# Kernel optimization log

Hardware: AMD Instinct MI355X
Metric: run time of the kernel (lower is better)

Reference implementation:

```python
import jax, jax.numpy as jnp
import numpy as np
from jax import lax

B, ROWS, COLS, K, LATENT = 8, 1536, 16, 32, 16
EPS_REG = 0.01  # torchsort regularization_strength
BIG = 1e30


def setup_inputs() -> dict:
    key = jax.random.key(0)
    ks = jax.random.split(key, 12)
    def w(k, shape):
        return (jax.random.normal(k, shape, jnp.float32) / np.sqrt(shape[0])).astype(jnp.float32)
    return {
        "table": jax.random.uniform(ks[0], (B, ROWS, COLS), jnp.float32),
        "enc_w1": w(ks[1], (COLS, 32)), "enc_b1": 0.01 * jax.random.normal(ks[2], (32,), jnp.float32),
        "enc_w2": w(ks[3], (32, 64)),   "enc_b2": 0.01 * jax.random.normal(ks[4], (64,), jnp.float32),
        "mean_w": w(ks[5], (64, LATENT)), "mean_b": 0.01 * jax.random.normal(ks[6], (LATENT,), jnp.float32),
        "dec_w1": w(ks[7], (LATENT, 32)), "dec_b1": 0.01 * jax.random.normal(ks[8], (32,), jnp.float32),
        "dec_w2": w(ks[9], (32, COLS)),   "dec_b2": 0.01 * jax.random.normal(ks[10], (COLS,), jnp.float32),
        "labels": jax.random.randint(ks[11], (ROWS,), 0, K, jnp.int32),
        "BlockSize": 64,
        "current_epoch": 0,
        "baseline": 0,
    }


def _soft_rank_l2(s, eps):
    # Exact soft_rank (Blondel et al. / torchsort, l2 reg, ascending):
    # project s/eps onto permutahedron of (n,...,1).
    n = s.shape[0]
    x = s / eps
    perm = jnp.argsort(-x)            # descending sort
    xs = x[perm]
    w = jnp.arange(n, 0, -1, dtype=x.dtype)
    # dual = non-increasing isotonic fit of y = xs - w == -iso_inc(-(xs - w))
    y = -(xs - w)
    S = jnp.concatenate([jnp.zeros((1,), x.dtype), jnp.cumsum(y)])
    idx = jnp.arange(n)
    length = jnp.maximum(idx[None, :] - idx[:, None] + 1, 1).astype(x.dtype)
    A = (S[1:][None, :] - S[:n][:, None]) / length           # mean(y[j..k])  [j,k]
    A = jnp.where(idx[None, :] >= idx[:, None], A, BIG)
    Bm = lax.cummin(A, axis=1, reverse=True)                  # min_{k>=i} A[j,k]
    Cm = lax.cummax(Bm, axis=0)                               # max_{j<=i} ...
    iso_inc = jnp.diagonal(Cm)
    dual = -iso_inc
    primal = xs - dual
    inv = jnp.argsort(perm)
    return primal[inv]


def _forward(table, enc_w1, enc_b1, enc_w2, enc_b2, mean_w, mean_b,
             dec_w1, dec_b1, dec_w2, dec_b2, labels, BlockSize):
    b = table.shape[0]
    # VAE (autoencoder path; z = latent mean)
    h = jax.nn.relu(table @ enc_w1 + enc_b1)
    h = jax.nn.relu(h @ enc_w2 + enc_b2)
    z = h @ mean_w + mean_b                                   # [B, rows, 16]
    r = jax.nn.relu(z @ dec_w1 + dec_b1)
    recon = jax.nn.relu(r @ dec_w2 + dec_b2)
    loss = jnp.mean((recon - table) ** 2)
    # clustering scores (labels fixed from batch 0, shared across batch)
    onehot = jax.nn.one_hot(labels, K, dtype=z.dtype)         # [rows, K]
    counts = jnp.maximum(onehot.sum(0), 1.0)                  # [K]
    centers = jnp.einsum('brd,rk->bkd', z, onehot) / counts[None, :, None]
    center_data = centers[:, labels, :]                       # gather back [B, rows, 16]
    d2 = jnp.mean((z - center_data) ** 2, axis=-1)            # [B, rows]
    mn = d2.min(axis=1, keepdims=True); mx = d2.max(axis=1, keepdims=True)
    d2 = (d2 - mn) / (mx - mn)
    scores = d2 + labels.astype(z.dtype)[None, :]
    # training branch
    smn = scores.min(axis=1, keepdims=True); smx = scores.max(axis=1, keepdims=True)
    scaled = (scores - smn) / (smx - smn) * jnp.asarray(b, z.dtype)  # * len(table)
    ranks = jax.vmap(lambda s: _soft_rank_l2(s, EPS_REG))(scaled)
    rank_idx = jnp.argsort(jnp.argsort(scores, axis=1), axis=1) // BlockSize + 1
    rows = table.shape[1]
    return (ranks.reshape(b, rows, 1), rank_idx.reshape(b, rows, 1),
            scores.reshape(b, rows, 1), loss)


def reference(table, enc_w1, enc_b1, enc_w2, enc_b2, mean_w, mean_b,
              dec_w1, dec_b1, dec_w2, dec_b2, labels, BlockSize,
              current_epoch, baseline):
    return _forward(table, enc_w1, enc_b1, enc_w2, enc_b2, mean_w, mean_b,
                    dec_w1, dec_b1, dec_w2, dec_b2, labels, BlockSize)
```

## Files before the change

### kernel.cpp

```cpp
#include <hip/hip_runtime.h>

#define BATCH 8
#define ROWS 1536
#define KCLS 32
#define NTOT (BATCH*ROWS)
#define ELEMS (NTOT*16)
#define SSTRIDE 3073
#define BIGF 1.0e30f

enum : int {
  WS_Z     = 0,
  WS_XS    = WS_Z + NTOT*16,
  WS_S     = WS_XS + NTOT,
  WS_DESC  = WS_S + BATCH*SSTRIDE,
  WS_ASCP  = WS_DESC + NTOT,
  WS_DSCP  = WS_ASCP + 4*NTOT,
  WS_GPART = WS_DSCP + 4*NTOT,
  WS_LOSSP = WS_GPART + BATCH*96*512,
};
#define WS_CPART WS_GPART

#define LW1  0
#define LB1  512
#define LW2  544
#define LB2  2592
#define LMW  2656
#define LMB  3680
#define LDW1 3696
#define LDB1 4208
#define LDW2 4240
#define LDB2 4752
#define LTOT 4768

#define AX   0
#define AH1  16
#define AH2  48
#define AZ   112
#define AR1  128
#define AREC 144
#define ASTRIDE 164

#define RPB 16

template<int IN_BASE, int IN_N, int OUT_BASE, int OUT_PW, int OUT_TOT,
         int WOFF, int BOFF, bool RELU>
__device__ __forceinline__ void layerw(float* __restrict__ act,
                                       const float* __restrict__ wsh,
                                       int lrow, int fway)
{
  const int o0 = fway * OUT_PW;
  float a0[OUT_PW], a1[OUT_PW], a2[OUT_PW], a3[OUT_PW];
#pragma unroll
  for (int j = 0; j < OUT_PW; ++j) {
    a0[j] = wsh[BOFF + o0 + j];
    a1[j] = 0.f; a2[j] = 0.f; a3[j] = 0.f;
  }

  const float4* arow = reinterpret_cast<const float4*>(&act[lrow*ASTRIDE + IN_BASE]);
#pragma unroll
  for (int i4 = 0; i4 < IN_N/4; ++i4) {
    const float4 sv = arow[i4];
    const float* wp0 = &wsh[WOFF + (i4*4 + 0)*OUT_TOT + o0];
    const float* wp1 = &wsh[WOFF + (i4*4 + 1)*OUT_TOT + o0];
    const float* wp2 = &wsh[WOFF + (i4*4 + 2)*OUT_TOT + o0];
    const float* wp3 = &wsh[WOFF + (i4*4 + 3)*OUT_TOT + o0];
    if constexpr (OUT_PW == 1) {
      a0[0] = fmaf(sv.x, wp0[0], a0[0]);
      a1[0] = fmaf(sv.y, wp1[0], a1[0]);
      a2[0] = fmaf(sv.z, wp2[0], a2[0]);
      a3[0] = fmaf(sv.w, wp3[0], a3[0]);
    } else if constexpr (OUT_PW == 2) {
      const float2 w0 = *reinterpret_cast<const float2*>(wp0);
      const float2 w1 = *reinterpret_cast<const float2*>(wp1);
      const float2 w2 = *reinterpret_cast<const float2*>(wp2);
      const float2 w3 = *reinterpret_cast<const float2*>(wp3);
      a0[0] = fmaf(sv.x, w0.x, a0[0]); a0[1] = fmaf(sv.x, w0.y, a0[1]);
      a1[0] = fmaf(sv.y, w1.x, a1[0]); a1[1] = fmaf(sv.y, w1.y, a1[1]);
      a2[0] = fmaf(sv.z, w2.x, a2[0]); a2[1] = fmaf(sv.z, w2.y, a2[1]);
      a3[0] = fmaf(sv.w, w3.x, a3[0]); a3[1] = fmaf(sv.w, w3.y, a3[1]);
    } else {
#pragma unroll
      for (int q = 0; q < OUT_PW/4; ++q) {
        const float4 w0 = reinterpret_cast<const float4*>(wp0)[q];
        const float4 w1 = reinterpret_cast<const float4*>(wp1)[q];
        const float4 w2 = reinterpret_cast<const float4*>(wp2)[q];
        const float4 w3 = reinterpret_cast<const float4*>(wp3)[q];
        a0[q*4+0] = fmaf(sv.x, w0.x, a0[q*4+0]);
        a0[q*4+1] = fmaf(sv.x, w0.y, a0[q*4+1]);
        a0[q*4+2] = fmaf(sv.x, w0.z, a0[q*4+2]);
        a0[q*4+3] = fmaf(sv.x, w0.w, a0[q*4+3]);
        a1[q*4+0] = fmaf(sv.y, w1.x, a1[q*4+0]);
        a1[q*4+1] = fmaf(sv.y, w1.y, a1[q*4+1]);
        a1[q*4+2] = fmaf(sv.y, w1.z, a1[q*4+2]);
        a1[q*4+3] = fmaf(sv.y, w1.w, a1[q*4+3]);
        a2[q*4+0] = fmaf(sv.z, w2.x, a2[q*4+0]);
        a2[q*4+1] = fmaf(sv.z, w2.y, a2[q*4+1]);
        a2[q*4+2] = fmaf(sv.z, w2.z, a2[q*4+2]);
        a2[q*4+3] = fmaf(sv.z, w2.w, a2[q*4+3]);
        a3[q*4+0] = fmaf(sv.w, w3.x, a3[q*4+0]);
        a3[q*4+1] = fmaf(sv.w, w3.y, a3[q*4+1]);
        a3[q*4+2] = fmaf(sv.w, w3.z, a3[q*4+2]);
        a3[q*4+3] = fmaf(sv.w, w3.w, a3[q*4+3]);
      }
    }
  }

  float* orow = &act[lrow*ASTRIDE + OUT_BASE + o0];
  if constexpr (OUT_PW == 1) {
    float v = (a0[0] + a1[0]) + (a2[0] + a3[0]);
    orow[0] = RELU ? fmaxf(v, 0.f) : v;
  } else if constexpr (OUT_PW == 2) {
    float2 v;
    v.x = (a0[0] + a1[0]) + (a2[0] + a3[0]);
    v.y = (a0[1] + a1[1]) + (a2[1] + a3[1]);
    if (RELU) { v.x = fmaxf(v.x, 0.f); v.y = fmaxf(v.y, 0.f); }
    *reinterpret_cast<float2*>(orow) = v;
  } else {
#pragma unroll
    for (int q = 0; q < OUT_PW/4; ++q) {
      float4 v;
      v.x = (a0[q*4+0] + a1[q*4+0]) + (a2[q*4+0] + a3[q*4+0]);
      v.y = (a0[q*4+1] + a1[q*4+1]) + (a2[q*4+1] + a3[q*4+1]);
      v.z = (a0[q*4+2] + a1[q*4+2]) + (a2[q*4+2] + a3[q*4+2]);
      v.w = (a0[q*4+3] + a1[q*4+3]) + (a2[q*4+3] + a3[q*4+3]);
      if (RELU) {
        v.x = fmaxf(v.x, 0.f); v.y = fmaxf(v.y, 0.f);
        v.z = fmaxf(v.z, 0.f); v.w = fmaxf(v.w, 0.f);
      }
      reinterpret_cast<float4*>(orow)[q] = v;
    }
  }
}

__global__ __launch_bounds__(256, 4) void k1_ae(
    const float* __restrict__ table,
    const float* __restrict__ w1, const float* __restrict__ b1,
    const float* __restrict__ w2, const float* __restrict__ b2,
    const float* __restrict__ mw, const float* __restrict__ mb,
    const float* __restrict__ dw1, const float* __restrict__ db1,
    const float* __restrict__ dw2, const float* __restrict__ db2,
    const int* __restrict__ labels,
    float* __restrict__ ws)
{
  const int tid  = threadIdx.x;
  const int lrow = tid & (RPB-1);
  const int fway = tid >> 4;
  const int blk  = blockIdx.x;
  const int b    = blk / 96;
  const int ch   = blk % 96;

  __shared__ float wsh[LTOT];
  __shared__ float act[RPB * ASTRIDE];
  __shared__ int   lbl[RPB];
  __shared__ float lred[4];

  {
    float4* d4 = reinterpret_cast<float4*>(wsh);
#define CPY(off, src, nf4) \
    { const float4* p = reinterpret_cast<const float4*>(src); \
      for (int t = tid; t < (nf4); t += 256) d4[(off)/4 + t] = p[t]; }
    CPY(LW1,  w1,  128) CPY(LB1,  b1,  8)  CPY(LW2,  w2,  512)
    CPY(LB2,  b2,  16)  CPY(LMW,  mw,  256) CPY(LMB,  mb,  4)
    CPY(LDW1, dw1, 128) CPY(LDB1, db1, 8)  CPY(LDW2, dw2, 128)
    CPY(LDB2, db2, 4)
#undef CPY
    if (tid < RPB) lbl[tid] = labels[ch * RPB + tid];
    if (tid < RPB*4) {
      const float4 v = reinterpret_cast<const float4*>(table)[blk*(RPB*4) + tid];
      reinterpret_cast<float4*>(act)[(tid >> 2)*(ASTRIDE/4) + (tid & 3)] = v;
    }
  }
  __syncthreads();

  layerw<AX,  16, AH1, 2, 32, LW1,  LB1,  true >(act, wsh, lrow, fway);
  __syncthreads();
  layerw<AH1, 32, AH2, 4, 64, LW2,  LB2,  true >(act, wsh, lrow, fway);
  __syncthreads();
  layerw<AH2, 64, AZ,  1, 16, LMW,  LMB,  false>(act, wsh, lrow, fway);
  __syncthreads();

  if (tid < RPB*4) {
    const float4 zv =
      reinterpret_cast<const float4*>(act)[(tid >> 2)*(ASTRIDE/4) + (AZ/4) + (tid & 3)];
    reinterpret_cast<float4*>(ws + WS_Z)[blk*(RPB*4) + tid] = zv;
  }

  layerw<AZ,  16, AR1, 2, 32, LDW1, LDB1, true >(act, wsh, lrow, fway);
  __syncthreads();
  layerw<AR1, 32, AREC,1, 16, LDW2, LDB2, true >(act, wsh, lrow, fway);
  __syncthreads();

  {
    const float d = act[lrow*ASTRIDE + AREC + fway] - act[lrow*ASTRIDE + AX + fway];
    float ls = d * d;
    for (int off = 32; off > 0; off >>= 1) ls += __shfl_down(ls, off);
    if ((tid & 63) == 0) lred[tid >> 6] = ls;
    __syncthreads();
    if (tid == 0) ws[WS_LOSSP + blk] = (lred[0] + lred[1]) + (lred[2] + lred[3]);
  }

  {
    float a0 = 0.f, a1 = 0.f;
    const int d0 = tid & 15, k0 = tid >> 4;
    const int k1c = k0 + 16;
#pragma unroll
    for (int rr = 0; rr < RPB; ++rr) {
      const int lb = lbl[rr];
      const float zv = act[rr*ASTRIDE + AZ + d0];
      a0 += (lb == k0)  ? zv : 0.f;
      a1 += (lb == k1c) ? zv : 0.f;
    }
    ws[WS_CPART + (b*96 + ch)*512 + tid]       = a0;
    ws[WS_CPART + (b*96 + ch)*512 + 256 + tid] = a1;
  }
}

__global__ __launch_bounds__(256) void kcount(const int* __restrict__ labels,
                                              float* __restrict__ ws,
                                              float* __restrict__ out)
{
  const int bi = blockIdx.x;
  const int jb = bi & 3, rb = (bi >> 2) % 6, b = bi / 24;
  const int tid = threadIdx.x;

  alignas(16) __shared__ float s_l[ROWS];
  __shared__ float cent[512];
  __shared__ float rmn[256], rmx[256];
  __shared__ int cnt[KCLS];

  if (tid < KCLS) cnt[tid] = 0;
  __syncthreads();

  int lbv[6];
#pragma unroll
  for (int c = 0; c < 6; ++c) {
    lbv[c] = labels[c*256 + tid];
    atomicAdd(&cnt[lbv[c]], 1);
  }

  float s1a = 0.f, s1b = 0.f, s2a = 0.f, s2b = 0.f;
  {
    const float* cp = ws + WS_CPART + (b*96)*512;
#pragma unroll 4
    for (int c = 0; c < 96; c += 2) {
      s1a += cp[c*512 + tid];
      s1b += cp[(c+1)*512 + tid];
      s2a += cp[c*512 + 256 + tid];
      s2b += cp[(c+1)*512 + 256 + tid];
    }
  }
  __syncthreads();
  {
    int cn1 = cnt[tid >> 4];         cn1 = cn1 > 1 ? cn1 : 1;
    int cn2 = cnt[(tid + 256) >> 4]; cn2 = cn2 > 1 ? cn2 : 1;
    cent[tid]       = (s1a + s1b) / (float)cn1;
    cent[tid + 256] = (s2a + s2b) / (float)cn2;
  }
  __syncthreads();

  float dv[6];
  float tmn = 3.0e38f, tmx = -3.0e38f;
#pragma unroll
  for (int c = 0; c < 6; ++c) {
    const int r = c*256 + tid;
    const float4* zp = reinterpret_cast<const float4*>(ws + WS_Z + (b*ROWS + r)*16);
    const float4* cq = reinterpret_cast<const float4*>(&cent[lbv[c]*16]);
    float s = 0.f;
#pragma unroll
    for (int q = 0; q < 4; ++q) {
      float4 zv = zp[q], cv = cq[q];
      float d0 = zv.x - cv.x, d1 = zv.y - cv.y, d2_ = zv.z - cv.z, d3 = zv.w - cv.w;
      s += d0*d0 + d1*d1 + d2_*d2_ + d3*d3;
    }
    dv[c] = s / 16.f;
    tmn = fminf(tmn, dv[c]); tmx = fmaxf(tmx, dv[c]);
  }
  rmn[tid] = tmn; rmx[tid] = tmx;
  __syncthreads();
  for (int off = 128; off > 0; off >>= 1) {
    if (tid < off) {
      rmn[tid] = fminf(rmn[tid], rmn[tid + off]);
      rmx[tid] = fmaxf(rmx[tid], rmx[tid + off]);
    }
    __syncthreads();
  }
  const float mn = rmn[0], mx = rmx[0];

#pragma unroll
  for (int c = 0; c < 6; ++c) {
    const int r = c*256 + tid;
    const float sc = (dv[c] - mn) / (mx - mn) + (float)lbv[c];
    s_l[r] = sc;
    if (jb == 0 && c == rb) out[2*NTOT + b*ROWS + r] = sc;
  }
  __syncthreads();

  const int r0 = rb*256 + tid;
  const float si = s_l[r0];
  int asc = 0, dsc = 0;
  const int j0 = jb*384;
  const float4* s4p = reinterpret_cast<const float4*>(&s_l[j0]);
#pragma unroll 4
  for (int kk = 0; kk < 96; ++kk) {
    const float4 s4 = s4p[kk];
    const int j = j0 + kk*4;
    const bool t0 = (s4.x == si && j   < r0);
    const bool t1 = (s4.y == si && j+1 < r0);
    const bool t2 = (s4.z == si && j+2 < r0);
    const bool t3 = (s4.w == si && j+3 < r0);
    asc += (s4.x < si || t0) ? 1 : 0;
    asc += (s4.y < si || t1) ? 1 : 0;
    asc += (s4.z < si || t2) ? 1 : 0;
    asc += (s4.w < si || t3) ? 1 : 0;
    dsc += (s4.x > si || t0) ? 1 : 0;
    dsc += (s4.y > si || t1) ? 1 : 0;
    dsc += (s4.z > si || t2) ? 1 : 0;
    dsc += (s4.w > si || t3) ? 1 : 0;
  }
  int* wsi = reinterpret_cast<int*>(ws);
  wsi[WS_ASCP + jb*NTOT + b*ROWS + r0] = asc;
  wsi[WS_DSCP + jb*NTOT + b*ROWS + r0] = dsc;

  if (bi == 0) {
    __syncthreads();
    rmn[tid] = ws[WS_LOSSP + tid] + ws[WS_LOSSP + 256 + tid] + ws[WS_LOSSP + 512 + tid];
    __syncthreads();
    for (int off = 128; off > 0; off >>= 1) {
      if (tid < off) rmn[tid] += rmn[tid + off];
      __syncthreads();
    }
    if (tid == 0) out[3*NTOT] = rmn[0] / (float)ELEMS;
  }
}

__global__ __launch_bounds__(256) void k67(const int* __restrict__ bsp,
                                           float* __restrict__ ws,
                                           float* __restrict__ out)
{
  const int b = blockIdx.x, tid = threadIdx.x;
  const int lane = tid & 63, wav = tid >> 6;
  __shared__ float xs_l[ROWS];
  __shared__ float rmn[256], rmx[256];
  __shared__ float wtot[4];
  const int* wsi = reinterpret_cast<const int*>(ws);
  int* wsw = reinterpret_cast<int*>(ws);
  const int BS = *bsp;

  int dscv[6];
  float sv[6];
  float tmn = 3.0e38f, tmx = -3.0e38f;
#pragma unroll
  for (int c = 0; c < 6; ++c) {
    const int r = c*256 + tid;
    const int idx = b*ROWS + r;
    int asc = 0, dsc = 0;
#pragma unroll
    for (int jb = 0; jb < 4; ++jb) {
      asc += wsi[WS_ASCP + jb*NTOT + idx];
      dsc += wsi[WS_DSCP + jb*NTOT + idx];
    }
    out[NTOT + idx] = (float)(asc / BS + 1);
    wsw[WS_DESC + idx] = dsc;
    dscv[c] = dsc;
    const float sc = out[2*NTOT + idx];
    sv[c] = sc;
    tmn = fminf(tmn, sc); tmx = fmaxf(tmx, sc);
  }
  rmn[tid] = tmn; rmx[tid] = tmx;
  __syncthreads();
  for (int off = 128; off > 0; off >>= 1) {
    if (tid < off) {
      rmn[tid] = fminf(rmn[tid], rmn[tid + off]);
      rmx[tid] = fmaxf(rmx[tid], rmx[tid + off]);
    }
    __syncthreads();
  }
  const float smn = rmn[0], smx = rmx[0];
  __syncthreads();

#pragma unroll
  for (int c = 0; c < 6; ++c) {
    const float scl = (sv[c] - smn) / (smx - smn) * 8.0f;
    xs_l[dscv[c]] = scl / 0.01f;
  }
  __syncthreads();

  const int base = tid * 6;
  float y[6], own = 0.f;
#pragma unroll
  for (int u = 0; u < 6; ++u) {
    ws[WS_XS + b*ROWS + base + u] = xs_l[base + u];
    y[u] = (float)(ROWS - (base + u)) - xs_l[base + u];
    own += y[u];
  }
  float v = own;
#pragma unroll
  for (int d = 1; d < 64; d <<= 1) {
    float o = __shfl_up(v, d);
    if (lane >= d) v += o;
  }
  if (lane == 63) wtot[wav] = v;
  __syncthreads();
  float wpre = 0.f;
  for (int w = 0; w < wav; ++w) wpre += wtot[w];
  float run = wpre + (v - own);
  float* S = ws + WS_S + b*SSTRIDE;
#pragma unroll
  for (int u = 0; u < 6; ++u) { S[base + u] = run; run += y[u]; }
  if (tid == 255) S[ROWS] = run;
#pragma unroll
  for (int u = 0; u < 6; ++u) S[ROWS + 1 + tid*6 + u] = BIGF;
}

__global__ __launch_bounds__(256) void k8a(float* __restrict__ ws)
{
  const int bi = blockIdx.x;
  const int c = bi & 7, ib = (bi >> 3) % 6, b = bi / 48;
  const int tid = threadIdx.x;
  __shared__ float Sseg[448];
  __shared__ float invl[192];
  const float* S = ws + WS_S + b*SSTRIDE;
  const int ibase = ib*256;
  const int segbase = ibase + c*192 + 1;
  Sseg[tid] = S[segbase + tid];
  if (tid < 192) {
    Sseg[256 + tid] = S[segbase + 256 + tid];
    invl[tid] = 1.0f / (float)(c*192 + tid + 1);
  }
  __syncthreads();
  const int i = ibase + tid;
  const float Si = S[i];
  float gm = 3.0e38f;
#pragma unroll 8
  for (int k = 0; k < 192; ++k)
    gm = fminf(gm, (Sseg[tid + k] - Si) * invl[k]);
  ws[WS_GPART + (b*8 + c)*ROWS + i] = gm;
}

__global__ __launch_bounds__(768) void k8b(float* __restrict__ ws,
                                           float* __restrict__ out)
{
  const int b = blockIdx.x, tid = threadIdx.x;
  const int lane = tid & 63, wav = tid >> 6;
  __shared__ float g[ROWS];
  __shared__ float wtot[12];
  for (int t = tid; t < ROWS; t += 768) {
    float gm = 3.0e38f;
#pragma unroll
    for (int c = 0; c < 8; ++c)
      gm = fminf(gm, ws[WS_GPART + (b*8 + c)*ROWS + t]);
    g[t] = gm;
  }
  __syncthreads();
  const float a = g[2*tid], cc = g[2*tid + 1];
  float v = fmaxf(a, cc);
#pragma unroll
  for (int d = 1; d < 64; d <<= 1) {
    float o = __shfl_up(v, d);
    if (lane >= d) v = fmaxf(v, o);
  }
  if (lane == 63) wtot[wav] = v;
  __syncthreads();
  float wpre = -3.0e38f;
  for (int w = 0; w < wav; ++w) wpre = fmaxf(wpre, wtot[w]);
  float lex = __shfl_up(v, 1);
  if (lane == 0) lex = -3.0e38f;
  const float excl = fmaxf(wpre, lex);
  const float i0 = fmaxf(excl, a);
  const float i1 = fmaxf(i0, cc);
  g[2*tid] = i0; g[2*tid + 1] = i1;
  __syncthreads();
  const float* xs = ws + WS_XS + b*ROWS;
  const int* desc = reinterpret_cast<const int*>(ws) + WS_DESC + b*ROWS;
  for (int t = tid; t < ROWS; t += 768) {
    const int dr = desc[t];
    out[b*ROWS + t] = xs[dr] + g[dr];
  }
}

extern "C" void kernel_launch(void* const* d_in, const int* in_sizes, int n_in,
                              void* d_out, int out_size, void* d_ws, size_t ws_size,
                              hipStream_t stream) {
  const float* table = (const float*)d_in[0];
  const float* w1  = (const float*)d_in[1];
  const float* b1  = (const float*)d_in[2];
  const float* w2  = (const float*)d_in[3];
  const float* b2  = (const float*)d_in[4];
  const float* mw  = (const float*)d_in[5];
  const float* mb  = (const float*)d_in[6];
  const float* dw1 = (const float*)d_in[7];
  const float* db1 = (const float*)d_in[8];
  const float* dw2 = (const float*)d_in[9];
  const float* db2 = (const float*)d_in[10];
  const int* labels = (const int*)d_in[11];
  const int* bsp    = (const int*)d_in[12];
  float* out = (float*)d_out;
  float* ws  = (float*)d_ws;

  k1_ae<<<768, 256, 0, stream>>>(table, w1, b1, w2, b2, mw, mb, dw1, db1, dw2, db2, labels, ws);
  kcount<<<192, 256, 0, stream>>>(labels, ws, out);
  k67<<<8, 256, 0, stream>>>(bsp, ws, out);
  k8a<<<384, 256, 0, stream>>>(ws);
  k8b<<<8, 768, 0, stream>>>(ws, out);
}
```

Before: 62.01 us.

## Fuse rank counting with scatter and move prefix-sum into segment-min kernel

Removes the 8-block k67 kernel. The rank-counting kernel now has each block handle 64 rows, with 4 lanes per row splitting the comparison range and combining counts through wave shuffles. It computes the scores min/max itself and writes rank_idx and the sorted scaled scores directly. The cumulative-sum array S is no longer stored in global memory; every k8a block rebuilds it in LDS from the sorted values. This saves one low-parallelism launch and its global round trips, at the cost of redundant prefix-sum work repeated across the 48 k8a blocks per batch and an extra min/max reduction in kranks.

```diff
diff --git a/kernel.cpp b/kernel.cpp
--- a/kernel.cpp
+++ b/kernel.cpp
@@ -5,17 +5,13 @@
 #define KCLS 32
 #define NTOT (BATCH*ROWS)
 #define ELEMS (NTOT*16)
-#define SSTRIDE 3073
 #define BIGF 1.0e30f
 
 enum : int {
   WS_Z     = 0,
   WS_XS    = WS_Z + NTOT*16,
-  WS_S     = WS_XS + NTOT,
-  WS_DESC  = WS_S + BATCH*SSTRIDE,
-  WS_ASCP  = WS_DESC + NTOT,
-  WS_DSCP  = WS_ASCP + 4*NTOT,
-  WS_GPART = WS_DSCP + 4*NTOT,
+  WS_DESC  = WS_XS + NTOT,
+  WS_GPART = WS_DESC + NTOT,
   WS_LOSSP = WS_GPART + BATCH*96*512,
 };
 #define WS_CPART WS_GPART
@@ -215,12 +211,13 @@
   }
 }
 
-__global__ __launch_bounds__(256) void kcount(const int* __restrict__ labels,
+__global__ __launch_bounds__(256) void kranks(const int* __restrict__ labels,
+                                              const int* __restrict__ bsp,
                                               float* __restrict__ ws,
                                               float* __restrict__ out)
 {
   const int bi = blockIdx.x;
-  const int jb = bi & 3, rb = (bi >> 2) % 6, b = bi / 24;
+  const int rg = bi % 24, b = bi / 24;
   const int tid = threadIdx.x;
 
   alignas(16) __shared__ float s_l[ROWS];
@@ -285,85 +282,15 @@
     __syncthreads();
   }
   const float mn = rmn[0], mx = rmx[0];
-
+  __syncthreads();
+
+  tmn = 3.0e38f; tmx = -3.0e38f;
 #pragma unroll
   for (int c = 0; c < 6; ++c) {
     const int r = c*256 + tid;
     const float sc = (dv[c] - mn) / (mx - mn) + (float)lbv[c];
     s_l[r] = sc;
-    if (jb == 0 && c == rb) out[2*NTOT + b*ROWS + r] = sc;
-  }
-  __syncthreads();
-
-  const int r0 = rb*256 + tid;
-  const float si = s_l[r0];
-  int asc = 0, dsc = 0;
-  const int j0 = jb*384;
-  const float4* s4p = reinterpret_cast<const float4*>(&s_l[j0]);
-#pragma unroll 4
-  for (int kk = 0; kk < 96; ++kk) {
-    const float4 s4 = s4p[kk];
-    const int j = j0 + kk*4;
-    const bool t0 = (s4.x == si && j   < r0);
-    const bool t1 = (s4.y == si && j+1 < r0);
-    const bool t2 = (s4.z == si && j+2 < r0);
-    const bool t3 = (s4.w == si && j+3 < r0);
-    asc += (s4.x < si || t0) ? 1 : 0;
-    asc += (s4.y < si || t1) ? 1 : 0;
-    asc += (s4.z < si || t2) ? 1 : 0;
-    asc += (s4.w < si || t3) ? 1 : 0;
-    dsc += (s4.x > si || t0) ? 1 : 0;
-    dsc += (s4.y > si || t1) ? 1 : 0;
-    dsc += (s4.z > si || t2) ? 1 : 0;
-    dsc += (s4.w > si || t3) ? 1 : 0;
-  }
-  int* wsi = reinterpret_cast<int*>(ws);
-  wsi[WS_ASCP + jb*NTOT + b*ROWS + r0] = asc;
-  wsi[WS_DSCP + jb*NTOT + b*ROWS + r0] = dsc;
-
-  if (bi == 0) {
-    __syncthreads();
-    rmn[tid] = ws[WS_LOSSP + tid] + ws[WS_LOSSP + 256 + tid] + ws[WS_LOSSP + 512 + tid];
-    __syncthreads();
-    for (int off = 128; off > 0; off >>= 1) {
-      if (tid < off) rmn[tid] += rmn[tid + off];
-      __syncthreads();
-    }
-    if (tid == 0) out[3*NTOT] = rmn[0] / (float)ELEMS;
-  }
-}
-
-__global__ __launch_bounds__(256) void k67(const int* __restrict__ bsp,
-                                           float* __restrict__ ws,
-                                           float* __restrict__ out)
-{
-  const int b = blockIdx.x, tid = threadIdx.x;
-  const int lane = tid & 63, wav = tid >> 6;
-  __shared__ float xs_l[ROWS];
-  __shared__ float rmn[256], rmx[256];
-  __shared__ float wtot[4];
-  const int* wsi = reinterpret_cast<const int*>(ws);
-  int* wsw = reinterpret_cast<int*>(ws);
-  const int BS = *bsp;
-
-  int dscv[6];
-  float sv[6];
-  float tmn = 3.0e38f, tmx = -3.0e38f;
-#pragma unroll
-  for (int c = 0; c < 6; ++c) {
-    const int r = c*256 + tid;
-    const int idx = b*ROWS + r;
-    int asc = 0, dsc = 0;
-#pragma unroll
-    for (int jb = 0; jb < 4; ++jb) {
-      asc += wsi[WS_ASCP + jb*NTOT + idx];
-      dsc += wsi[WS_DSCP + jb*NTOT + idx];
-    }
-    out[NTOT + idx] = (float)(asc / BS + 1);
-    wsw[WS_DESC + idx] = dsc;
-    dscv[c] = dsc;
-    const float sc = out[2*NTOT + idx];
-    sv[c] = sc;
+    if (c*4 + (tid >> 6) == rg) out[2*NTOT + b*ROWS + r] = sc;
     tmn = fminf(tmn, sc); tmx = fmaxf(tmx, sc);
   }
   rmn[tid] = tmn; rmx[tid] = tmx;
@@ -376,40 +303,53 @@
     __syncthreads();
   }
   const float smn = rmn[0], smx = rmx[0];
-  __syncthreads();
-
-#pragma unroll
-  for (int c = 0; c < 6; ++c) {
-    const float scl = (sv[c] - smn) / (smx - smn) * 8.0f;
-    xs_l[dscv[c]] = scl / 0.01f;
-  }
-  __syncthreads();
-
-  const int base = tid * 6;
-  float y[6], own = 0.f;
-#pragma unroll
-  for (int u = 0; u < 6; ++u) {
-    ws[WS_XS + b*ROWS + base + u] = xs_l[base + u];
-    y[u] = (float)(ROWS - (base + u)) - xs_l[base + u];
-    own += y[u];
-  }
-  float v = own;
-#pragma unroll
-  for (int d = 1; d < 64; d <<= 1) {
-    float o = __shfl_up(v, d);
-    if (lane >= d) v += o;
-  }
-  if (lane == 63) wtot[wav] = v;
-  __syncthreads();
-  float wpre = 0.f;
-  for (int w = 0; w < wav; ++w) wpre += wtot[w];
-  float run = wpre + (v - own);
-  float* S = ws + WS_S + b*SSTRIDE;
-#pragma unroll
-  for (int u = 0; u < 6; ++u) { S[base + u] = run; run += y[u]; }
-  if (tid == 255) S[ROWS] = run;
-#pragma unroll
-  for (int u = 0; u < 6; ++u) S[ROWS + 1 + tid*6 + u] = BIGF;
+
+  const int row_local = tid >> 2, q = tid & 3;
+  const int r0 = rg*64 + row_local;
+  const float si = s_l[r0];
+  int asc = 0, dsc = 0;
+  {
+    const int j0 = q*384;
+    const float4* s4p = reinterpret_cast<const float4*>(&s_l[j0]);
+#pragma unroll 4
+    for (int kk = 0; kk < 96; ++kk) {
+      const float4 s4 = s4p[kk];
+      const int j = j0 + kk*4;
+      const bool t0 = (s4.x == si && j   < r0);
+      const bool t1 = (s4.y == si && j+1 < r0);
+      const bool t2 = (s4.z == si && j+2 < r0);
+      const bool t3 = (s4.w == si && j+3 < r0);
+      asc += (s4.x < si || t0) ? 1 : 0;
+      asc += (s4.y < si || t1) ? 1 : 0;
+      asc += (s4.z < si || t2) ? 1 : 0;
+      asc += (s4.w < si || t3) ? 1 : 0;
+      dsc += (s4.x > si || t0) ? 1 : 0;
+      dsc += (s4.y > si || t1) ? 1 : 0;
+      dsc += (s4.z > si || t2) ? 1 : 0;
+      dsc += (s4.w > si || t3) ? 1 : 0;
+    }
+  }
+  asc += __shfl_xor(asc, 1); asc += __shfl_xor(asc, 2);
+  dsc += __shfl_xor(dsc, 1); dsc += __shfl_xor(dsc, 2);
+  if (q == 0) {
+    const int BS = *bsp;
+    const int idx = b*ROWS + r0;
+    out[NTOT + idx] = (float)(asc / BS + 1);
+    reinterpret_cast<int*>(ws)[WS_DESC + idx] = dsc;
+    const float scl = (si - smn) / (smx - smn) * 8.0f;
+    ws[WS_XS + b*ROWS + dsc] = scl / 0.01f;
+  }
+
+  if (bi == 0) {
+    __syncthreads();
+    rmn[tid] = ws[WS_LOSSP + tid] + ws[WS_LOSSP + 256 + tid] + ws[WS_LOSSP + 512 + tid];
+    __syncthreads();
+    for (int off = 128; off > 0; off >>= 1) {
+      if (tid < off) rmn[tid] += rmn[tid + off];
+      __syncthreads();
+    }
+    if (tid == 0) out[3*NTOT] = rmn[0] / (float)ELEMS;
+  }
 }
 
 __global__ __launch_bounds__(256) void k8a(float* __restrict__ ws)
@@ -417,24 +357,49 @@
   const int bi = blockIdx.x;
   const int c = bi & 7, ib = (bi >> 3) % 6, b = bi / 48;
   const int tid = threadIdx.x;
-  __shared__ float Sseg[448];
+  const int lane = tid & 63, wav = tid >> 6;
+
+  __shared__ float S[3073];
   __shared__ float invl[192];
-  const float* S = ws + WS_S + b*SSTRIDE;
+  __shared__ float wtot[4];
+
+  {
+    const int base = tid * 6;
+    const float* xs = ws + WS_XS + b*ROWS;
+    float y[6], own = 0.f;
+#pragma unroll
+    for (int u = 0; u < 6; ++u) {
+      y[u] = (float)(ROWS - (base + u)) - xs[base + u];
+      own += y[u];
+    }
+    float v = own;
+#pragma unroll
+    for (int d = 1; d < 64; d <<= 1) {
+      float o = __shfl_up(v, d);
+      if (lane >= d) v += o;
+    }
+    if (lane == 63) wtot[wav] = v;
+    __syncthreads();
+    float wpre = 0.f;
+    for (int w = 0; w < wav; ++w) wpre += wtot[w];
+    float run = wpre + (v - own);
+#pragma unroll
+    for (int u = 0; u < 6; ++u) { S[base + u] = run; run += y[u]; }
+    if (tid == 255) S[ROWS] = run;
+#pragma unroll
+    for (int u = 0; u < 6; ++u) S[ROWS + 1 + base + u] = BIGF;
+    if (tid < 192) invl[tid] = 1.0f / (float)(c*192 + tid + 1);
+  }
+  __syncthreads();
+
   const int ibase = ib*256;
   const int segbase = ibase + c*192 + 1;
-  Sseg[tid] = S[segbase + tid];
-  if (tid < 192) {
-    Sseg[256 + tid] = S[segbase + 256 + tid];
-    invl[tid] = 1.0f / (float)(c*192 + tid + 1);
-  }
-  __syncthreads();
-  const int i = ibase + tid;
-  const float Si = S[i];
+  const float Si = S[ibase + tid];
   float gm = 3.0e38f;
 #pragma unroll 8
   for (int k = 0; k < 192; ++k)
-    gm = fminf(gm, (Sseg[tid + k] - Si) * invl[k]);
-  ws[WS_GPART + (b*8 + c)*ROWS + i] = gm;
+    gm = fminf(gm, (S[segbase + tid + k] - Si) * invl[k]);
+  ws[WS_GPART + (b*8 + c)*ROWS + ibase + tid] = gm;
 }
 
 __global__ __launch_bounds__(768) void k8b(float* __restrict__ ws,
@@ -498,8 +463,7 @@
   float* ws  = (float*)d_ws;
 
   k1_ae<<<768, 256, 0, stream>>>(table, w1, b1, w2, b2, mw, mb, dw1, db1, dw2, db2, labels, ws);
-  kcount<<<192, 256, 0, stream>>>(labels, ws, out);
-  k67<<<8, 256, 0, stream>>>(bsp, ws, out);
+  kranks<<<192, 256, 0, stream>>>(labels, bsp, ws, out);
   k8a<<<384, 256, 0, stream>>>(ws);
   k8b<<<8, 768, 0, stream>>>(ws, out);
 }
```

New measurement: 56.74 us. 1.09x faster.
